# Performance work log

Hardware: AMD Instinct MI355X
Metric: run time of the kernel (lower is better)

Reference implementation:

```python
import jax, jax.numpy as jnp
import numpy as np

N_HEADS = 16
D_K = 64
MAX_LEN = 5000


def setup_inputs() -> dict:
    key = jax.random.key(0)
    ks = jax.random.split(key, 6)
    B, L, D = 4, 1024, 1024
    s = 1.0 / np.sqrt(D).astype(np.float32)
    return {
        "x": jax.random.normal(ks[0], (B, L, D), jnp.float32),
        "W_q": jax.random.normal(ks[1], (D, D), jnp.float32) * s,
        "b_q": jnp.zeros((D,), jnp.float32),
        "W_k": jax.random.normal(ks[2], (D, D), jnp.float32) * s,
        "b_k": jnp.zeros((D,), jnp.float32),
        "W_v": jax.random.normal(ks[3], (D, D), jnp.float32) * s,
        "b_v": jnp.zeros((D,), jnp.float32),
        "W_o": jax.random.normal(ks[4], (D, D), jnp.float32) * s,
        "b_o": jnp.zeros((D,), jnp.float32),
        "Er": jax.random.normal(ks[5], (MAX_LEN, D_K), jnp.float32) * 0.02,
    }


def reference(x, W_q, b_q, W_k, b_k, W_v, b_v, W_o, b_o, Er):
    B, L, D = x.shape
    H = N_HEADS
    dk = D // H
    # torch nn.Linear: y = x @ W.T + b
    Q = (x @ W_q.T + b_q).reshape(B, L, H, dk).transpose(0, 2, 1, 3)  # (B,H,L,dk)
    K = (x @ W_k.T + b_k).reshape(B, L, H, dk).transpose(0, 2, 1, 3)
    V = (x @ W_v.T + b_v).reshape(B, L, H, dk).transpose(0, 2, 1, 3)
    AC = jnp.einsum('bhid,bhjd->bhij', Q, K)  # (B,H,L,L)
    rel_pos = jnp.arange(L - 1, -L, -1) + (MAX_LEN - 1)  # (2L-1,)
    # mode='clip' matches intended math: clamped rows fall in the part that
    # the relative shift slices away.
    Er_embed = jnp.take(Er, rel_pos, axis=0, mode='clip')  # (2L-1, dk)
    BD = jnp.einsum('bhid,rd->bhir', Q, Er_embed)  # (B,H,L,2L-1)
    # _relative_shift: view is a no-op (shape already (B,H,L,2L-1)), then slice
    BD = BD[..., L - 1:]  # (B,H,L,L)
    scores = (AC + BD) / np.sqrt(dk).astype(np.float32)
    attn = jax.nn.softmax(scores, axis=-1)
    out = jnp.einsum('bhij,bhjd->bhid', attn, V)
    out = out.transpose(0, 2, 1, 3).reshape(B, L, D)
    return out @ W_o.T + b_o
```

## Files before the change

### kernel.cpp

```cpp
#include <hip/hip_runtime.h>
#include <cstdint>
#include <cstddef>


typedef __attribute__((ext_vector_type(8))) short short8;
typedef __attribute__((ext_vector_type(4))) float f32x4;

#define MFMA_BF16(a, b, c) __builtin_amdgcn_mfma_f32_16x16x32_bf16((a), (b), (c), 0, 0, 0)

constexpr int kB = 4, kL = 1024, kD = 1024, kH = 16;
constexpr int kBL = kB * kL;
constexpr float kScale = 0.125f * 1.44269504088896340736f;

static __device__ __forceinline__ unsigned short f32_to_bf16(float f) {
  union { float f; uint32_t u; } c; c.f = f;
  uint32_t u = c.u + 0x7fffu + ((c.u >> 16) & 1u);
  return (unsigned short)(u >> 16);
}

static __device__ __forceinline__ void gload_lds16(const void* g, void* l) {
  __builtin_amdgcn_global_load_lds(
      (const __attribute__((address_space(1))) void*)g,
      (__attribute__((address_space(3))) void*)l, 16, 0, 0);
}

__global__ __launch_bounds__(256)
void cast_all(const float* __restrict__ x,  const float* __restrict__ Wq,
              const float* __restrict__ Wk, const float* __restrict__ Wv,
              const float* __restrict__ Wo,
              unsigned short* __restrict__ xb, unsigned short* __restrict__ Wcat,
              unsigned short* __restrict__ Wob) {
  int i = blockIdx.x * blockDim.x + threadIdx.x;
  const float* src;
  ushort4* dst;
  int off;
  if (i < 1048576) {
    src = x; dst = reinterpret_cast<ushort4*>(xb); off = i;
  } else {
    int j = i - 1048576;
    int seg = j >> 18;
    off = j & 262143;
    if (seg == 0)      { src = Wq; dst = reinterpret_cast<ushort4*>(Wcat); }
    else if (seg == 1) { src = Wk; dst = reinterpret_cast<ushort4*>(Wcat) + 262144; }
    else if (seg == 2) { src = Wv; dst = reinterpret_cast<ushort4*>(Wcat) + 524288; }
    else               { src = Wo; dst = reinterpret_cast<ushort4*>(Wob); }
  }
  float4 v = reinterpret_cast<const float4*>(src)[off];
  ushort4 o;
  o.x = f32_to_bf16(v.x); o.y = f32_to_bf16(v.y);
  o.z = f32_to_bf16(v.z); o.w = f32_to_bf16(v.w);
  dst[off] = o;
}

__global__ __launch_bounds__(512, 2)
void gemm_qkv(const unsigned short* __restrict__ A,
              const unsigned short* __restrict__ Bm,
              const float* __restrict__ bq, const float* __restrict__ bk,
              const float* __restrict__ bv,
              const float* __restrict__ Er,
              unsigned short* __restrict__ Qh, unsigned short* __restrict__ Kh,
              unsigned short* __restrict__ Vth) {
  __shared__ __align__(16) char smem[131072];
  const int tid  = threadIdx.x;
  const int lane = tid & 63, wave = tid >> 6;
  const int quad = lane >> 4, l15 = lane & 15, lhalf = l15 >> 1;
  const int wr = wave >> 2, wc = wave & 3;

  const int bid = blockIdx.x;
  const int xcd = bid & 7, idx = bid >> 3;
  const int mt_ = idx / 6, nt_ = idx - mt_ * 6;
  const int m0 = ((xcd >> 1) * 4 + mt_) * 256;
  const int n0 = ((xcd & 1) * 6 + nt_) * 256;

  const int lane_off = (l15 & 1) * 64 + ((quad * 16) ^ ((lhalf & 3) << 4));
  const int aoff = lhalf * 128 + lane_off + wr * 8192;
  const int boff = lhalf * 128 + lane_off + wc * 4096;

  int srow[2], scol[2];
#pragma unroll
  for (int j = 0; j < 2; ++j) {
    int poff = (j * 512 + tid) * 16;
    int L = poff ^ (((poff >> 7) & 3) << 4);
    srow[j] = ((L >> 7) << 1) | ((L >> 6) & 1);
    scol[j] = (L & 63) >> 1;
  }

  auto stageAB = [&](int X, int kh, int tt) {
    const unsigned short* src = X ? Bm : A;
    const int rbase = X ? n0 : m0;
    char* dst = smem + ((tt & 1) * 65536 + X * 32768 + kh * 16384) + tid * 16;
    const int kc = tt * 64 + kh * 32;
#pragma unroll
    for (int j = 0; j < 2; ++j)
      gload_lds16(src + (size_t)(rbase + srow[j]) * 1024 + kc + scol[j],
                  dst + j * 8192);
  };

  const f32x4 vzero = {0.f, 0.f, 0.f, 0.f};
  f32x4 acc[8][4];
#pragma unroll
  for (int i = 0; i < 8; ++i)
#pragma unroll
    for (int j = 0; j < 4; ++j) acc[i][j] = vzero;

  stageAB(0, 0, 0); stageAB(1, 0, 0); stageAB(0, 1, 0); stageAB(1, 1, 0);
  stageAB(0, 0, 1); stageAB(1, 0, 1);
  asm volatile("s_waitcnt vmcnt(4)" ::: "memory");
  __builtin_amdgcn_s_barrier();

#define LDA(KH, MB) do {                                                      \
    _Pragma("unroll")                                                         \
    for (int f_ = 0; f_ < 4; ++f_)                                            \
      af[f_] = *(const short8*)(RA + (KH) * 16384 + aoff + ((MB) + f_) * 1024); \
  } while (0)
#define LDB(KH) do {                                                          \
    _Pragma("unroll")                                                         \
    for (int n_ = 0; n_ < 4; ++n_)                                            \
      bf[n_] = *(const short8*)(RB + (KH) * 16384 + boff + n_ * 1024);        \
  } while (0)
#define BARA() do {                                                           \
    __builtin_amdgcn_s_barrier();                                             \
    asm volatile("s_waitcnt lgkmcnt(0)" ::: "memory");                        \
    __builtin_amdgcn_sched_barrier(0);                                        \
  } while (0)
#define MFMA_QUAD(MB) do {                                                    \
    __builtin_amdgcn_s_setprio(1);                                            \
    _Pragma("unroll")                                                         \
    for (int mq_ = 0; mq_ < 4; ++mq_) {                                       \
      _Pragma("unroll")                                                       \
      for (int nq_ = 0; nq_ < 4; ++nq_)                                       \
        acc[(MB) + mq_][nq_] =                                                \
            MFMA_BF16(af[mq_], bf[nq_], acc[(MB) + mq_][nq_]);                \
    }                                                                         \
    __builtin_amdgcn_s_setprio(0);                                            \
  } while (0)

  for (int t = 0; t < 16; ++t) {
    const char* RA = smem + (t & 1) * 65536;
    const char* RB = RA + 32768;
    short8 af[4], bf[4];
    LDA(0, 0); LDB(0);
    if (t + 1 < 16) stageAB(0, 1, t + 1);
    BARA(); MFMA_QUAD(0);
    __builtin_amdgcn_s_barrier();
    LDA(0, 4);
    if (t + 1 < 16) stageAB(1, 1, t + 1);
    BARA(); MFMA_QUAD(4);
    __builtin_amdgcn_s_barrier();
    LDA(1, 0); LDB(1);
    if (t + 2 < 16) stageAB(0, 0, t + 2);
    BARA(); MFMA_QUAD(0);
    __builtin_amdgcn_s_barrier();
    LDA(1, 4);
    if (t + 2 < 16) stageAB(1, 0, t + 2);
    BARA(); MFMA_QUAD(4);
    if (t < 14) asm volatile("s_waitcnt vmcnt(4)" ::: "memory");
    else        asm volatile("s_waitcnt vmcnt(0)" ::: "memory");
    __builtin_amdgcn_s_barrier();
  }

#undef LDA
#undef LDB
#undef BARA
#undef MFMA_QUAD

  const int wsel = n0 >> 10;
  const int gmb  = m0 + wr * 128;
  const int bb   = gmb >> 10, i0l = gmb & 1023;
  const int nl0  = (n0 & 1023) + wc * 64;
  const int hh   = nl0 >> 6;
  const size_t bh = (size_t)(bb * 16 + hh);

  if (wsel == 0) {
#pragma unroll
    for (int mf = 0; mf < 8; ++mf)
#pragma unroll
      for (int nf = 0; nf < 4; ++nf)
#pragma unroll
        for (int r = 0; r < 4; ++r) {
          const int i = i0l + mf * 16 + quad * 4 + r;
          const int n = nl0 + nf * 16 + l15;
          float v = (acc[mf][nf][r] + bq[n]) * kScale;
          Qh[(bh * 1024 + i) * 64 + (n & 63)] = f32_to_bf16(v);
        }
  } else if (wsel == 1) {
#pragma unroll
    for (int mf = 0; mf < 8; ++mf)
#pragma unroll
      for (int nf = 0; nf < 4; ++nf)
#pragma unroll
        for (int r = 0; r < 4; ++r) {
          const int i = i0l + mf * 16 + quad * 4 + r;
          const int n = nl0 + nf * 16 + l15;
          const int d = n & 63;
          float v = acc[mf][nf][r] + bk[n] + Er[(size_t)(4999 - i) * 64 + d];
          Kh[(bh * 1024 + i) * 64 + d] = f32_to_bf16(v);
        }
  } else {
    __syncthreads();
    unsigned short* W = (unsigned short*)smem + (size_t)wave * 8192;
#pragma unroll
    for (int mf = 0; mf < 8; ++mf)
#pragma unroll
      for (int nf = 0; nf < 4; ++nf) {
        ushort4 pk;
        const int n = nl0 + nf * 16 + l15;
        pk.x = f32_to_bf16(acc[mf][nf][0] + bv[n]);
        pk.y = f32_to_bf16(acc[mf][nf][1] + bv[n]);
        pk.z = f32_to_bf16(acc[mf][nf][2] + bv[n]);
        pk.w = f32_to_bf16(acc[mf][nf][3] + bv[n]);
        *(ushort4*)&W[(size_t)(nf * 16 + l15) * 128 + mf * 16 + quad * 4] = pk;
      }
#pragma unroll
    for (int p = 0; p < 16; ++p) {
      const int u = p * 64 + lane;
      const int d = u >> 4, ch = (u & 15) * 8;
      short8 vv = *(const short8*)&W[(size_t)d * 128 + ch];
      *(short8*)&Vth[(bh * 64 + d) * 1024 + i0l + ch] = vv;
    }
  }
}

__global__ __launch_bounds__(256)
void gemm_out(const unsigned short* __restrict__ A,
              const unsigned short* __restrict__ Bm,
              const float* __restrict__ bias,
              float* __restrict__ outf) {
  __shared__ unsigned short As[2][128 * 32];
  __shared__ unsigned short Bs[2][64 * 32];
  const int tid  = threadIdx.x;
  const int lane = tid & 63, wave = tid >> 6;
  const int quad = lane >> 4, l15 = lane & 15;
  const int m0 = blockIdx.y * 128, n0 = blockIdx.x * 64;
  const int K = 1024;

  const f32x4 vzero = {0.f, 0.f, 0.f, 0.f};
  f32x4 acc[2][4];
#pragma unroll
  for (int i = 0; i < 2; ++i)
#pragma unroll
    for (int j = 0; j < 4; ++j) acc[i][j] = vzero;

  for (int k0 = 0; k0 < K; k0 += 64) {
    __syncthreads();
#pragma unroll
    for (int j = 0; j < 4; ++j) {
      int u = j * 256 + tid;
      int half = u >> 9, row = (u >> 2) & 127, c = (u & 3) * 8 + half * 32;
      gload_lds16(A + (size_t)(m0 + row) * K + k0 + c, (char*)&As[0][0] + (size_t)u * 16);
    }
#pragma unroll
    for (int j = 0; j < 2; ++j) {
      int u = j * 256 + tid;
      int half = u >> 8, row = (u >> 2) & 63, c = (u & 3) * 8 + half * 32;
      gload_lds16(Bm + (size_t)(n0 + row) * K + k0 + c, (char*)&Bs[0][0] + (size_t)u * 16);
    }
    __syncthreads();

#pragma unroll
    for (int ks = 0; ks < 2; ++ks) {
      short8 af[2], bfv[4];
#pragma unroll
      for (int mt = 0; mt < 2; ++mt)
        af[mt] = *(const short8*)&As[ks][(wave * 32 + mt * 16 + l15) * 32 + quad * 8];
#pragma unroll
      for (int nt = 0; nt < 4; ++nt)
        bfv[nt] = *(const short8*)&Bs[ks][(nt * 16 + l15) * 32 + quad * 8];
#pragma unroll
      for (int mt = 0; mt < 2; ++mt)
#pragma unroll
        for (int nt = 0; nt < 4; ++nt)
          acc[mt][nt] = MFMA_BF16(af[mt], bfv[nt], acc[mt][nt]);
    }
  }

#pragma unroll
  for (int mt = 0; mt < 2; ++mt)
#pragma unroll
    for (int nt = 0; nt < 4; ++nt)
#pragma unroll
      for (int r = 0; r < 4; ++r) {
        const int gm = m0 + wave * 32 + mt * 16 + quad * 4 + r;
        const int gn = n0 + nt * 16 + l15;
        outf[(size_t)gm * 1024 + gn] = acc[mt][nt][r] + bias[gn];
      }
}

__global__ __launch_bounds__(256)
void attn_kernel(const unsigned short* __restrict__ Q,
                 const unsigned short* __restrict__ Kp,
                 const unsigned short* __restrict__ Vt,
                 unsigned short* __restrict__ Ao) {
  __shared__ unsigned short Ks[2][2][64 * 32];
  __shared__ unsigned short Vs[2][2][64 * 32];
  __shared__ unsigned short Plds[4][32 * 72];
  const int tid  = threadIdx.x;
  const int lane = tid & 63, wave = tid >> 6;
  const int quad = lane >> 4, l15 = lane & 15;
  const int bh = blockIdx.x;
  const int qb = blockIdx.y;
  const size_t base  = (size_t)bh * (kL * 64);
  const size_t vbase = (size_t)bh * (64 * kL);
  const int i0 = qb * 128 + wave * 32;

  short8 qf[2][2];
#pragma unroll
  for (int mt = 0; mt < 2; ++mt)
#pragma unroll
    for (int ks = 0; ks < 2; ++ks)
      qf[mt][ks] = *(const short8*)
          &Q[base + (size_t)(i0 + mt * 16 + l15) * 64 + ks * 32 + quad * 8];

  auto stage = [&](int buf, int kb) {
#pragma unroll
    for (int j = 0; j < 2; ++j) {
      int u = j * 256 + tid;
      int half = u >> 8, row = (u >> 2) & 63, c = (u & 3) * 8;
      gload_lds16(Kp + base + (size_t)(kb * 64 + row) * 64 + half * 32 + c,
                  (char*)&Ks[buf][0][0] + (size_t)u * 16);
      gload_lds16(Vt + vbase + (size_t)row * kL + kb * 64 + half * 32 + c,
                  (char*)&Vs[buf][0][0] + (size_t)u * 16);
    }
  };

  const f32x4 vzero = {0.f, 0.f, 0.f, 0.f};
  f32x4 of[2][4];
#pragma unroll
  for (int mt = 0; mt < 2; ++mt)
#pragma unroll
    for (int dt = 0; dt < 4; ++dt) of[mt][dt] = vzero;
  float lsum[2][4] = {{0.f, 0.f, 0.f, 0.f}, {0.f, 0.f, 0.f, 0.f}};

  unsigned short* Pw = Plds[wave];

  stage(0, 0);
  __syncthreads();

  for (int kb = 0; kb < 16; ++kb) {
    const int cur = kb & 1, nxt = cur ^ 1;
    if (kb < 15) stage(nxt, kb + 1);

    short8 kf[4][2];
#pragma unroll
    for (int nt = 0; nt < 4; ++nt)
#pragma unroll
      for (int ks = 0; ks < 2; ++ks)
        kf[nt][ks] = *(const short8*)&Ks[cur][ks][(nt * 16 + l15) * 32 + quad * 8];
    f32x4 sf[2][4];
#pragma unroll
    for (int mt = 0; mt < 2; ++mt)
#pragma unroll
      for (int nt = 0; nt < 4; ++nt) {
        sf[mt][nt] = MFMA_BF16(qf[mt][0], kf[nt][0], vzero);
        sf[mt][nt] = MFMA_BF16(qf[mt][1], kf[nt][1], sf[mt][nt]);
      }

#pragma unroll
    for (int mt = 0; mt < 2; ++mt)
#pragma unroll
      for (int nt = 0; nt < 4; ++nt)
#pragma unroll
        for (int r = 0; r < 4; ++r) {
          float p = __builtin_amdgcn_exp2f(sf[mt][nt][r]);
          lsum[mt][r] += p;
          union { float f; uint32_t u; } c; c.f = p;
          Pw[(mt * 16 + quad * 4 + r) * 72 + nt * 16 + l15] =
              (unsigned short)((c.u + 0x8000u) >> 16);
        }
    short8 pf[2][2];
#pragma unroll
    for (int mt = 0; mt < 2; ++mt)
#pragma unroll
      for (int ks = 0; ks < 2; ++ks)
        pf[mt][ks] = *(const short8*)&Pw[(mt * 16 + l15) * 72 + ks * 32 + quad * 8];

    short8 vf[4][2];
#pragma unroll
    for (int dt = 0; dt < 4; ++dt)
#pragma unroll
      for (int ks = 0; ks < 2; ++ks)
        vf[dt][ks] = *(const short8*)&Vs[cur][ks][(dt * 16 + l15) * 32 + quad * 8];
#pragma unroll
    for (int mt = 0; mt < 2; ++mt)
#pragma unroll
      for (int dt = 0; dt < 4; ++dt) {
        of[mt][dt] = MFMA_BF16(pf[mt][0], vf[dt][0], of[mt][dt]);
        of[mt][dt] = MFMA_BF16(pf[mt][1], vf[dt][1], of[mt][dt]);
      }

    __syncthreads();
  }

#pragma unroll
  for (int mask = 1; mask < 16; mask <<= 1)
#pragma unroll
    for (int mt = 0; mt < 2; ++mt)
#pragma unroll
      for (int r = 0; r < 4; ++r)
        lsum[mt][r] += __shfl_xor(lsum[mt][r], mask);
  float rl[2][4];
#pragma unroll
  for (int mt = 0; mt < 2; ++mt)
#pragma unroll
    for (int r = 0; r < 4; ++r) rl[mt][r] = __builtin_amdgcn_rcpf(lsum[mt][r]);

  const int b = bh >> 4, h = bh & 15;
#pragma unroll
  for (int mt = 0; mt < 2; ++mt)
#pragma unroll
    for (int dt = 0; dt < 4; ++dt)
#pragma unroll
      for (int r = 0; r < 4; ++r) {
        const int ig = i0 + mt * 16 + quad * 4 + r;
        float v = of[mt][dt][r] * rl[mt][r];
        Ao[((size_t)(b * 1024 + ig)) * 1024 + h * 64 + dt * 16 + l15] = f32_to_bf16(v);
      }
}

extern "C" void kernel_launch(void* const* d_in, const int* in_sizes, int n_in,
                              void* d_out, int out_size, void* d_ws, size_t ws_size,
                              hipStream_t stream) {
  const float* x   = (const float*)d_in[0];
  const float* W_q = (const float*)d_in[1];
  const float* b_q = (const float*)d_in[2];
  const float* W_k = (const float*)d_in[3];
  const float* b_k = (const float*)d_in[4];
  const float* W_v = (const float*)d_in[5];
  const float* b_v = (const float*)d_in[6];
  const float* W_o = (const float*)d_in[7];
  const float* b_o = (const float*)d_in[8];
  const float* Er  = (const float*)d_in[9];
  float* out = (float*)d_out;

  char* ws = (char*)d_ws;
  unsigned short* xb   = (unsigned short*)(ws + (size_t)0);
  unsigned short* Wcat = (unsigned short*)(ws + ((size_t)8  << 20));
  unsigned short* Wob  = (unsigned short*)(ws + ((size_t)14 << 20));
  unsigned short* Qh   = (unsigned short*)(ws + ((size_t)16 << 20));
  unsigned short* Kh   = (unsigned short*)(ws + ((size_t)24 << 20));
  unsigned short* Vth  = (unsigned short*)(ws + ((size_t)32 << 20));
  unsigned short* Aoh  = (unsigned short*)(ws + ((size_t)40 << 20));

  cast_all<<<8192, 256, 0, stream>>>(x, W_q, W_k, W_v, W_o, xb, Wcat, Wob);

  gemm_qkv<<<192, 512, 0, stream>>>(
      xb, Wcat, b_q, b_k, b_v, Er, Qh, Kh, Vth);

  attn_kernel<<<dim3(kB * kH, kL / 128), 256, 0, stream>>>(Qh, Kh, Vth, Aoh);

  gemm_out<<<dim3(16, 32), 256, 0, stream>>>(Aoh, Wob, b_o, out);
}
```

Before: 175.6 us.

## Pipeline and swizzle out-projection GEMM, transpose score MFMA, relax QKV waitcnts

```diff
diff --git a/kernel.cpp b/kernel.cpp
--- a/kernel.cpp
+++ b/kernel.cpp
@@ -16,6 +16,11 @@
   union { float f; uint32_t u; } c; c.f = f;
   uint32_t u = c.u + 0x7fffu + ((c.u >> 16) & 1u);
   return (unsigned short)(u >> 16);
+}
+
+static __device__ __forceinline__ uint32_t pack_bf16x2(float a, float b) {
+  union { float f; uint32_t u; } ca, cb; ca.f = a; cb.f = b;
+  return ((ca.u + 0x8000u) >> 16) | ((cb.u + 0x8000u) & 0xffff0000u);
 }
 
 static __device__ __forceinline__ void gload_lds16(const void* g, void* l) {
@@ -146,6 +151,8 @@
     LDA(0, 4);
     if (t + 1 < 16) stageAB(1, 1, t + 1);
     BARA(); MFMA_QUAD(4);
+    if (t < 15) asm volatile("s_waitcnt vmcnt(8)" ::: "memory");
+    else        asm volatile("s_waitcnt vmcnt(0)" ::: "memory");
     __builtin_amdgcn_s_barrier();
     LDA(1, 0); LDB(1);
     if (t + 2 < 16) stageAB(0, 0, t + 2);
@@ -154,8 +161,9 @@
     LDA(1, 4);
     if (t + 2 < 16) stageAB(1, 0, t + 2);
     BARA(); MFMA_QUAD(4);
-    if (t < 14) asm volatile("s_waitcnt vmcnt(4)" ::: "memory");
-    else        asm volatile("s_waitcnt vmcnt(0)" ::: "memory");
+    if (t < 14)       asm volatile("s_waitcnt vmcnt(8)" ::: "memory");
+    else if (t == 14) asm volatile("s_waitcnt vmcnt(4)" ::: "memory");
+    else              asm volatile("s_waitcnt vmcnt(0)" ::: "memory");
     __builtin_amdgcn_s_barrier();
   }
 
@@ -226,13 +234,52 @@
               const unsigned short* __restrict__ Bm,
               const float* __restrict__ bias,
               float* __restrict__ outf) {
-  __shared__ unsigned short As[2][128 * 32];
-  __shared__ unsigned short Bs[2][64 * 32];
+  __shared__ __align__(16) char smem[49152];
   const int tid  = threadIdx.x;
   const int lane = tid & 63, wave = tid >> 6;
   const int quad = lane >> 4, l15 = lane & 15;
   const int m0 = blockIdx.y * 128, n0 = blockIdx.x * 64;
-  const int K = 1024;
+
+  const int afo = (l15 >> 1) * 128 + (l15 & 1) * 64 +
+                  ((quad * 16) ^ (((l15 >> 1) & 3) << 4));
+
+  int arow[4], acol[4], akh[4];
+#pragma unroll
+  for (int j = 0; j < 4; ++j) {
+    int u = j * 256 + tid;
+    akh[j] = u >> 9;
+    int poff = (u & 511) * 16;
+    int L = poff ^ (((poff >> 7) & 3) << 4);
+    arow[j] = ((L >> 7) << 1) | ((L >> 6) & 1);
+    acol[j] = (L & 63) >> 1;
+  }
+  int brow[2], bcol[2], bkh[2];
+#pragma unroll
+  for (int j = 0; j < 2; ++j) {
+    int u = j * 256 + tid;
+    bkh[j] = u >> 8;
+    int poff = (u & 255) * 16;
+    int L = poff ^ (((poff >> 7) & 3) << 4);
+    brow[j] = ((L >> 7) << 1) | ((L >> 6) & 1);
+    bcol[j] = (L & 63) >> 1;
+  }
+
+  auto stageG = [&](int buf, int t) {
+    char* base = smem + buf * 24576;
+    const int kc = t * 64;
+#pragma unroll
+    for (int j = 0; j < 4; ++j) {
+      int u = j * 256 + tid;
+      gload_lds16(A + (size_t)(m0 + arow[j]) * 1024 + kc + akh[j] * 32 + acol[j],
+                  base + u * 16);
+    }
+#pragma unroll
+    for (int j = 0; j < 2; ++j) {
+      int u = j * 256 + tid;
+      gload_lds16(Bm + (size_t)(n0 + brow[j]) * 1024 + kc + bkh[j] * 32 + bcol[j],
+                  base + 16384 + u * 16);
+    }
+  };
 
   const f32x4 vzero = {0.f, 0.f, 0.f, 0.f};
   f32x4 acc[2][4];
@@ -241,37 +288,33 @@
 #pragma unroll
     for (int j = 0; j < 4; ++j) acc[i][j] = vzero;
 
-  for (int k0 = 0; k0 < K; k0 += 64) {
-    __syncthreads();
-#pragma unroll
-    for (int j = 0; j < 4; ++j) {
-      int u = j * 256 + tid;
-      int half = u >> 9, row = (u >> 2) & 127, c = (u & 3) * 8 + half * 32;
-      gload_lds16(A + (size_t)(m0 + row) * K + k0 + c, (char*)&As[0][0] + (size_t)u * 16);
-    }
-#pragma unroll
-    for (int j = 0; j < 2; ++j) {
-      int u = j * 256 + tid;
-      int half = u >> 8, row = (u >> 2) & 63, c = (u & 3) * 8 + half * 32;
-      gload_lds16(Bm + (size_t)(n0 + row) * K + k0 + c, (char*)&Bs[0][0] + (size_t)u * 16);
-    }
-    __syncthreads();
-
+  stageG(0, 0);
+  for (int t = 0; t < 16; ++t) {
+    const int cur = t & 1;
+    if (t < 15) stageG(cur ^ 1, t + 1);
+    if (t < 15) asm volatile("s_waitcnt vmcnt(6)" ::: "memory");
+    else        asm volatile("s_waitcnt vmcnt(0)" ::: "memory");
+    __builtin_amdgcn_s_barrier();
+    __builtin_amdgcn_sched_barrier(0);
+    const char* Ab = smem + cur * 24576;
+    const char* Bb = Ab + 16384;
 #pragma unroll
     for (int ks = 0; ks < 2; ++ks) {
       short8 af[2], bfv[4];
 #pragma unroll
       for (int mt = 0; mt < 2; ++mt)
-        af[mt] = *(const short8*)&As[ks][(wave * 32 + mt * 16 + l15) * 32 + quad * 8];
+        af[mt] = *(const short8*)(Ab + ks * 8192 + wave * 2048 + mt * 1024 + afo);
 #pragma unroll
       for (int nt = 0; nt < 4; ++nt)
-        bfv[nt] = *(const short8*)&Bs[ks][(nt * 16 + l15) * 32 + quad * 8];
+        bfv[nt] = *(const short8*)(Bb + ks * 4096 + nt * 1024 + afo);
 #pragma unroll
       for (int mt = 0; mt < 2; ++mt)
 #pragma unroll
         for (int nt = 0; nt < 4; ++nt)
           acc[mt][nt] = MFMA_BF16(af[mt], bfv[nt], acc[mt][nt]);
     }
+    __builtin_amdgcn_s_barrier();
+    __builtin_amdgcn_sched_barrier(0);
   }
 
 #pragma unroll
@@ -329,7 +372,7 @@
   for (int mt = 0; mt < 2; ++mt)
 #pragma unroll
     for (int dt = 0; dt < 4; ++dt) of[mt][dt] = vzero;
-  float lsum[2][4] = {{0.f, 0.f, 0.f, 0.f}, {0.f, 0.f, 0.f, 0.f}};
+  float lsum[2] = {0.f, 0.f};
 
   unsigned short* Pw = Plds[wave];
 
@@ -351,22 +394,24 @@
     for (int mt = 0; mt < 2; ++mt)
 #pragma unroll
       for (int nt = 0; nt < 4; ++nt) {
-        sf[mt][nt] = MFMA_BF16(qf[mt][0], kf[nt][0], vzero);
-        sf[mt][nt] = MFMA_BF16(qf[mt][1], kf[nt][1], sf[mt][nt]);
+        sf[mt][nt] = MFMA_BF16(kf[nt][0], qf[mt][0], vzero);
+        sf[mt][nt] = MFMA_BF16(kf[nt][1], qf[mt][1], sf[mt][nt]);
       }
 
 #pragma unroll
     for (int mt = 0; mt < 2; ++mt)
 #pragma unroll
-      for (int nt = 0; nt < 4; ++nt)
-#pragma unroll
-        for (int r = 0; r < 4; ++r) {
-          float p = __builtin_amdgcn_exp2f(sf[mt][nt][r]);
-          lsum[mt][r] += p;
-          union { float f; uint32_t u; } c; c.f = p;
-          Pw[(mt * 16 + quad * 4 + r) * 72 + nt * 16 + l15] =
-              (unsigned short)((c.u + 0x8000u) >> 16);
-        }
+      for (int nt = 0; nt < 4; ++nt) {
+        float p0 = __builtin_amdgcn_exp2f(sf[mt][nt][0]);
+        float p1 = __builtin_amdgcn_exp2f(sf[mt][nt][1]);
+        float p2 = __builtin_amdgcn_exp2f(sf[mt][nt][2]);
+        float p3 = __builtin_amdgcn_exp2f(sf[mt][nt][3]);
+        lsum[mt] += (p0 + p1) + (p2 + p3);
+        uint2 w;
+        w.x = pack_bf16x2(p0, p1);
+        w.y = pack_bf16x2(p2, p3);
+        *(uint2*)&Pw[(mt * 16 + l15) * 72 + nt * 16 + quad * 4] = w;
+      }
     short8 pf[2][2];
 #pragma unroll
     for (int mt = 0; mt < 2; ++mt)
@@ -391,18 +436,16 @@
     __syncthreads();
   }
 
-#pragma unroll
-  for (int mask = 1; mask < 16; mask <<= 1)
-#pragma unroll
-    for (int mt = 0; mt < 2; ++mt)
-#pragma unroll
-      for (int r = 0; r < 4; ++r)
-        lsum[mt][r] += __shfl_xor(lsum[mt][r], mask);
   float rl[2][4];
 #pragma unroll
-  for (int mt = 0; mt < 2; ++mt)
-#pragma unroll
-    for (int r = 0; r < 4; ++r) rl[mt][r] = __builtin_amdgcn_rcpf(lsum[mt][r]);
+  for (int mt = 0; mt < 2; ++mt) {
+    float s = lsum[mt];
+    s += __shfl_xor(s, 16);
+    s += __shfl_xor(s, 32);
+#pragma unroll
+    for (int r = 0; r < 4; ++r)
+      rl[mt][r] = __builtin_amdgcn_rcpf(__shfl(s, quad * 4 + r));
+  }
 
   const int b = bh >> 4, h = bh & 15;
 #pragma unroll
```

Result: no change. 176.0 us (+0.2%).
